# Kernel tuning notes

Hardware: AMD Instinct MI355X
Metric: run time of the kernel (lower is better)

The kernel has to match this reference:

```python
import jax, jax.numpy as jnp
import numpy as np

N_NODES = 50000
N_GRAPHS = 512


def gcn_conv(x, W, b, row, col, norm, n_nodes):
    # PyG GCNConv: h = x @ W; out_i = sum_{j->i} norm_ij * h_j + b
    h = x @ W  # [N, H]
    msgs = h[row] * norm[:, None]  # gather source features, scale
    out = jax.ops.segment_sum(msgs, col, num_segments=n_nodes)
    return out + b


def reference(x, edge_index, batch, W0, b0, W1, b1, W2, b2, Wf, bf):
    n = x.shape[0]
    src, dst = edge_index[0], edge_index[1]
    # add self loops
    loop = jnp.arange(n)
    row = jnp.concatenate([src, loop])
    col = jnp.concatenate([dst, loop])
    # symmetric degree normalization: 1/sqrt(deg_i * deg_j)
    deg = jax.ops.segment_sum(jnp.ones_like(col, dtype=x.dtype), col, num_segments=n)
    dis = jnp.where(deg > 0, 1.0 / jnp.sqrt(deg), 0.0)
    norm = dis[row] * dis[col]

    h = x
    for W, b in ((W0, b0), (W1, b1), (W2, b2)):
        h = jax.nn.relu(gcn_conv(h, W, b, row, col, norm, n))
        # dropout is identity in eval mode

    # global mean pool over graphs
    sums = jax.ops.segment_sum(h, batch, num_segments=N_GRAPHS)
    counts = jax.ops.segment_sum(jnp.ones((n,), dtype=h.dtype), batch, num_segments=N_GRAPHS)
    pooled = sums / jnp.maximum(counts, 1.0)[:, None]  # [B, H]

    logits = pooled @ Wf + bf
    return jax.nn.log_softmax(logits, axis=1)


def setup_inputs() -> dict:
    key = jax.random.key(0)
    ks = jax.random.split(key, 12)
    d_in, d_h, d_out = 128, 128, 10
    x = jax.random.normal(ks[0], (N_NODES, d_in), dtype=jnp.float32)
    edge_index = jax.random.randint(ks[1], (2, 600000), 0, N_NODES, dtype=jnp.int64)
    batch = jnp.sort(jax.random.randint(ks[2], (N_NODES,), 0, N_GRAPHS, dtype=jnp.int64))
    s = 1.0 / np.sqrt(d_h)
    return {
        "x": x,
        "edge_index": edge_index,
        "batch": batch,
        "W0": jax.random.normal(ks[3], (d_in, d_h), dtype=jnp.float32) * s,
        "b0": jnp.zeros((d_h,), dtype=jnp.float32),
        "W1": jax.random.normal(ks[4], (d_h, d_h), dtype=jnp.float32) * s,
        "b1": jnp.zeros((d_h,), dtype=jnp.float32),
        "W2": jax.random.normal(ks[5], (d_h, d_h), dtype=jnp.float32) * s,
        "b2": jnp.zeros((d_h,), dtype=jnp.float32),
        "Wf": jax.random.normal(ks[6], (d_h, d_out), dtype=jnp.float32) * s,
        "bf": jnp.zeros((d_out,), dtype=jnp.float32),
    }
```

## Files before the change

kernel.cpp:

```cpp
#include <hip/hip_runtime.h>
#include <hip/hip_bf16.h>

#define NN 50000
#define NE 600000
#define NG 512
#define DH 128

__global__ __launch_bounds__(256) void k_zero(float* p, int n) {
    int i = blockIdx.x * 256 + threadIdx.x;
    if (i < n) p[i] = 0.0f;
}

__global__ __launch_bounds__(256) void k_hist(const int* __restrict__ dst, int* __restrict__ deg) {
    int e = blockIdx.x * 256 + threadIdx.x;
    if (e < NE) atomicAdd(&deg[dst[e]], 1);
}

__global__ __launch_bounds__(256) void k_counts(const int* __restrict__ batch, float* __restrict__ counts) {
    int i = blockIdx.x * 256 + threadIdx.x;
    if (i < NN) atomicAdd(&counts[batch[i]], 1.0f);
}

__global__ __launch_bounds__(256) void k_alloc(const int* __restrict__ deg, int* __restrict__ gcur,
                                               int* __restrict__ rowstart, int* __restrict__ cursor,
                                               float* __restrict__ dis) {
    int i = blockIdx.x * 256 + threadIdx.x;
    if (i >= NN) return;
    int d = deg[i];
    int st = atomicAdd(gcur, d);
    rowstart[i] = st;
    cursor[i] = st;
    dis[i] = 1.0f / sqrtf((float)(d + 1));
}

__global__ __launch_bounds__(256) void k_fill(const int* __restrict__ src, const int* __restrict__ dst,
                                              const float* __restrict__ dis, int* __restrict__ cursor,
                                              int* __restrict__ csrc, float* __restrict__ cw) {
    int e = blockIdx.x * 256 + threadIdx.x;
    if (e >= NE) return;
    int s = src[e], d = dst[e];
    int slot = atomicAdd(&cursor[d], 1);
    csrc[slot] = s;
    cw[slot] = dis[s] * dis[d];
}

__global__ __launch_bounds__(256) void k_gemm128(const float* __restrict__ A,
                                                 const float* __restrict__ W,
                                                 float* __restrict__ C, int M) {
    __shared__ float As[64][20];
    __shared__ float Bs[16][132];
    int tid = threadIdx.x;
    int r0 = blockIdx.x * 64;
    int tr = tid >> 4, tc = tid & 15;

    float acc[4][8];
#pragma unroll
    for (int i = 0; i < 4; ++i)
#pragma unroll
        for (int j = 0; j < 8; ++j) acc[i][j] = 0.f;

    int arow = tid >> 2, ac4 = (tid & 3) * 4;

    for (int k0 = 0; k0 < 128; k0 += 16) {
        float4 av = make_float4(0.f, 0.f, 0.f, 0.f);
        int gr = r0 + arow;
        if (gr < M) av = *(const float4*)&A[gr * 128 + k0 + ac4];
        *(float4*)&As[arow][ac4] = av;
#pragma unroll
        for (int t = 0; t < 2; ++t) {
            int idx = tid + t * 256;
            int bk = idx >> 5, bc4 = (idx & 31) * 4;
            *(float4*)&Bs[bk][bc4] = *(const float4*)&W[(k0 + bk) * 128 + bc4];
        }
        __syncthreads();
#pragma unroll
        for (int kk = 0; kk < 16; ++kk) {
            float a[4];
#pragma unroll
            for (int i = 0; i < 4; ++i) a[i] = As[tr * 4 + i][kk];
            float4 bv0 = *(float4*)&Bs[kk][tc * 8];
            float4 bv1 = *(float4*)&Bs[kk][tc * 8 + 4];
            float b[8] = {bv0.x, bv0.y, bv0.z, bv0.w, bv1.x, bv1.y, bv1.z, bv1.w};
#pragma unroll
            for (int i = 0; i < 4; ++i)
#pragma unroll
                for (int j = 0; j < 8; ++j) acc[i][j] = fmaf(a[i], b[j], acc[i][j]);
        }
        __syncthreads();
    }

#pragma unroll
    for (int i = 0; i < 4; ++i) {
        int gr = r0 + tr * 4 + i;
        if (gr < M) {
            float4 o0 = make_float4(acc[i][0], acc[i][1], acc[i][2], acc[i][3]);
            float4 o1 = make_float4(acc[i][4], acc[i][5], acc[i][6], acc[i][7]);
            *(float4*)&C[gr * 128 + tc * 8] = o0;
            *(float4*)&C[gr * 128 + tc * 8 + 4] = o1;
        }
    }
}

template <int POOL>
__global__ __launch_bounds__(256) void k_gather(const float* __restrict__ h,
                                                const int* __restrict__ rowstart,
                                                const int* __restrict__ rowend,
                                                const int* __restrict__ csrc,
                                                const float* __restrict__ cw,
                                                const float* __restrict__ dis,
                                                const float* __restrict__ bias,
                                                float* __restrict__ outbuf,
                                                const int* __restrict__ batch,
                                                float* __restrict__ sums) {
    int t = blockIdx.x * 256 + threadIdx.x;
    int node = t >> 5;
    if (node >= NN) return;
    int f4 = t & 31;

    float d = dis[node];
    float w0 = d * d;
    float4 hv = ((const float4*)h)[node * 32 + f4];
    float4 acc = make_float4(hv.x * w0, hv.y * w0, hv.z * w0, hv.w * w0);

    int s = rowstart[node];
    int e = rowend[node];
    for (; s < e; ++s) {
        int sn = csrc[s];
        float w = cw[s];
        float4 v = ((const float4*)h)[sn * 32 + f4];
        acc.x = fmaf(v.x, w, acc.x);
        acc.y = fmaf(v.y, w, acc.y);
        acc.z = fmaf(v.z, w, acc.z);
        acc.w = fmaf(v.w, w, acc.w);
    }

    float4 b = ((const float4*)bias)[f4];
    acc.x = fmaxf(acc.x + b.x, 0.f);
    acc.y = fmaxf(acc.y + b.y, 0.f);
    acc.z = fmaxf(acc.z + b.z, 0.f);
    acc.w = fmaxf(acc.w + b.w, 0.f);

    if (POOL == 0) {
        ((float4*)outbuf)[node * 32 + f4] = acc;
    } else {
        int g = batch[node];
        float* o = sums + g * 128 + f4 * 4;
        atomicAdd(o + 0, acc.x);
        atomicAdd(o + 1, acc.y);
        atomicAdd(o + 2, acc.z);
        atomicAdd(o + 3, acc.w);
    }
}

__global__ __launch_bounds__(64) void k_head(const float* __restrict__ sums,
                                             const float* __restrict__ counts,
                                             const float* __restrict__ Wf,
                                             const float* __restrict__ bf,
                                             float* __restrict__ out) {
    int g = blockIdx.x;
    int l = threadIdx.x;
    float inv = 1.0f / fmaxf(counts[g], 1.0f);
    float p0 = sums[g * 128 + l] * inv;
    float p1 = sums[g * 128 + 64 + l] * inv;
    float logit[10];
#pragma unroll
    for (int o = 0; o < 10; ++o) {
        float part = p0 * Wf[l * 10 + o] + p1 * Wf[(l + 64) * 10 + o];
#pragma unroll
        for (int s = 32; s > 0; s >>= 1) part += __shfl_xor(part, s);
        logit[o] = part + bf[o];
    }
    if (l == 0) {
        float m = logit[0];
#pragma unroll
        for (int o = 1; o < 10; ++o) m = fmaxf(m, logit[o]);
        float sum = 0.f;
#pragma unroll
        for (int o = 0; o < 10; ++o) sum += expf(logit[o] - m);
        float lse = m + logf(sum);
#pragma unroll
        for (int o = 0; o < 10; ++o) out[g * 10 + o] = logit[o] - lse;
    }
}

extern "C" void kernel_launch(void* const* d_in, const int* in_sizes, int n_in,
                              void* d_out, int out_size, void* d_ws, size_t ws_size,
                              hipStream_t stream) {
    const float* x     = (const float*)d_in[0];
    const int*   ei    = (const int*)d_in[1];
    const int*   batch = (const int*)d_in[2];
    const float* W0 = (const float*)d_in[3];
    const float* b0 = (const float*)d_in[4];
    const float* W1 = (const float*)d_in[5];
    const float* b1 = (const float*)d_in[6];
    const float* W2 = (const float*)d_in[7];
    const float* b2 = (const float*)d_in[8];
    const float* Wf = (const float*)d_in[9];
    const float* bf = (const float*)d_in[10];
    float* out = (float*)d_out;

    float* ws = (float*)d_ws;
    float* sums    = ws;
    float* counts  = ws + 65536;
    int*   in_deg  = (int*)(ws + 66048);
    int*   gcur    = (int*)(ws + 116096);
    float* dis     = ws + 116160;
    int*   rowstart= (int*)(ws + 166208);
    int*   cursor  = (int*)(ws + 216256);
    int*   csr_src = (int*)(ws + 266304);
    float* csr_w   = ws + 866368;
    float* bufA    = ws + 1466432;
    float* bufB    = bufA + NN * DH;

    const int* src = ei;
    const int* dst = ei + NE;

    k_zero<<<(116160 + 255) / 256, 256, 0, stream>>>(ws, 116160);
    k_hist<<<2344, 256, 0, stream>>>(dst, in_deg);
    k_counts<<<196, 256, 0, stream>>>(batch, counts);
    k_alloc<<<196, 256, 0, stream>>>(in_deg, gcur, rowstart, cursor, dis);
    k_fill<<<2344, 256, 0, stream>>>(src, dst, dis, cursor, csr_src, csr_w);

    k_gemm128<<<(NN + 63) / 64, 256, 0, stream>>>(x, W0, bufB, NN);
    k_gather<0><<<6250, 256, 0, stream>>>(bufB, rowstart, cursor, csr_src, csr_w, dis, b0, bufA, batch, sums);

    k_gemm128<<<(NN + 63) / 64, 256, 0, stream>>>(bufA, W1, bufB, NN);
    k_gather<0><<<6250, 256, 0, stream>>>(bufB, rowstart, cursor, csr_src, csr_w, dis, b1, bufA, batch, sums);

    k_gemm128<<<(NN + 63) / 64, 256, 0, stream>>>(bufA, W2, bufB, NN);
    k_gather<1><<<6250, 256, 0, stream>>>(bufB, rowstart, cursor, csr_src, csr_w, dis, b2, nullptr, batch, sums);

    k_head<<<512, 64, 0, stream>>>(sums, counts, Wf, bf, out);
}
```

Before: 446.0 us.

## Store activations in bf16 and use MFMA bf16 GEMMs for GCN layers

Converts the input features and weights to bf16, replaces the fp32 SIMT GEMM with a bf16 MFMA 16x16x32 kernel that loads operands straight from global memory, and stores the intermediate hidden features in bf16. The gather kernels read bf16 rows, which halves the bytes moved in the edge-gather phase, and accumulate in fp32. The cost is an extra conversion pass over x and the weights, reduced precision in the intermediate activations, and scattered 2-byte stores from the GEMM epilogue.

```diff
diff --git a/kernel.cpp b/kernel.cpp
--- a/kernel.cpp
+++ b/kernel.cpp
@@ -4,7 +4,22 @@
 #define NN 50000
 #define NE 600000
 #define NG 512
-#define DH 128
+
+typedef __attribute__((ext_vector_type(8))) short bf16x8;
+typedef __attribute__((ext_vector_type(4))) float f32x4;
+
+__device__ __forceinline__ float bf_lo(unsigned u) {
+    unsigned v = u << 16;
+    return __builtin_bit_cast(float, v);
+}
+__device__ __forceinline__ float bf_hi(unsigned u) {
+    unsigned v = u & 0xFFFF0000u;
+    return __builtin_bit_cast(float, v);
+}
+__device__ __forceinline__ unsigned f2bf(float f) {
+    unsigned u = __builtin_bit_cast(unsigned, f);
+    return (u + 0x7FFFu + ((u >> 16) & 1u)) >> 16;
+}
 
 __global__ __launch_bounds__(256) void k_zero(float* p, int n) {
     int i = blockIdx.x * 256 + threadIdx.x;
@@ -44,111 +59,122 @@
     cw[slot] = dis[s] * dis[d];
 }
 
-__global__ __launch_bounds__(256) void k_gemm128(const float* __restrict__ A,
-                                                 const float* __restrict__ W,
-                                                 float* __restrict__ C, int M) {
-    __shared__ float As[64][20];
-    __shared__ float Bs[16][132];
-    int tid = threadIdx.x;
-    int r0 = blockIdx.x * 64;
-    int tr = tid >> 4, tc = tid & 15;
-
-    float acc[4][8];
-#pragma unroll
-    for (int i = 0; i < 4; ++i)
-#pragma unroll
-        for (int j = 0; j < 8; ++j) acc[i][j] = 0.f;
-
-    int arow = tid >> 2, ac4 = (tid & 3) * 4;
-
-    for (int k0 = 0; k0 < 128; k0 += 16) {
-        float4 av = make_float4(0.f, 0.f, 0.f, 0.f);
-        int gr = r0 + arow;
-        if (gr < M) av = *(const float4*)&A[gr * 128 + k0 + ac4];
-        *(float4*)&As[arow][ac4] = av;
-#pragma unroll
-        for (int t = 0; t < 2; ++t) {
-            int idx = tid + t * 256;
-            int bk = idx >> 5, bc4 = (idx & 31) * 4;
-            *(float4*)&Bs[bk][bc4] = *(const float4*)&W[(k0 + bk) * 128 + bc4];
+__global__ __launch_bounds__(256) void k_cvt_x(const float4* __restrict__ in, uint2* __restrict__ out, int n4) {
+    int i = blockIdx.x * 256 + threadIdx.x;
+    if (i >= n4) return;
+    float4 v = in[i];
+    uint2 o;
+    o.x = f2bf(v.x) | (f2bf(v.y) << 16);
+    o.y = f2bf(v.z) | (f2bf(v.w) << 16);
+    out[i] = o;
+}
+
+__global__ __launch_bounds__(256) void k_cvt_w(const float* __restrict__ W0, const float* __restrict__ W1,
+                                               const float* __restrict__ W2, unsigned short* __restrict__ Wt) {
+    int idx = blockIdx.x * 256 + threadIdx.x;
+    if (idx >= 3 * 16384) return;
+    int m = idx >> 14;
+    int r = idx & 16383;
+    int k = r >> 7, c = r & 127;
+    const float* W = (m == 0) ? W0 : (m == 1) ? W1 : W2;
+    Wt[m * 16384 + c * 128 + k] = (unsigned short)f2bf(W[k * 128 + c]);
+}
+
+__global__ __launch_bounds__(256) void k_gemm_mfma(const unsigned short* __restrict__ A,
+                                                   const unsigned short* __restrict__ Wt,
+                                                   unsigned short* __restrict__ C, int M) {
+    int wave = threadIdx.x >> 6;
+    int lane = threadIdx.x & 63;
+    int rowbase = blockIdx.x * 64 + wave * 16;
+    int lr = lane & 15;
+    int kg = lane >> 4;
+
+    int arow = rowbase + lr;
+    if (arow >= M) arow = M - 1;
+    bf16x8 a[4];
+#pragma unroll
+    for (int kt = 0; kt < 4; ++kt)
+        a[kt] = *(const bf16x8*)&A[arow * 128 + kt * 32 + kg * 8];
+
+    f32x4 acc[8];
+#pragma unroll
+    for (int nt = 0; nt < 8; ++nt) acc[nt] = (f32x4){0.f, 0.f, 0.f, 0.f};
+
+#pragma unroll
+    for (int nt = 0; nt < 8; ++nt) {
+        const unsigned short* wp = &Wt[(nt * 16 + lr) * 128 + kg * 8];
+#pragma unroll
+        for (int kt = 0; kt < 4; ++kt) {
+            bf16x8 b = *(const bf16x8*)&wp[kt * 32];
+            acc[nt] = __builtin_amdgcn_mfma_f32_16x16x32_bf16(a[kt], b, acc[nt], 0, 0, 0);
         }
-        __syncthreads();
-#pragma unroll
-        for (int kk = 0; kk < 16; ++kk) {
-            float a[4];
-#pragma unroll
-            for (int i = 0; i < 4; ++i) a[i] = As[tr * 4 + i][kk];
-            float4 bv0 = *(float4*)&Bs[kk][tc * 8];
-            float4 bv1 = *(float4*)&Bs[kk][tc * 8 + 4];
-            float b[8] = {bv0.x, bv0.y, bv0.z, bv0.w, bv1.x, bv1.y, bv1.z, bv1.w};
-#pragma unroll
-            for (int i = 0; i < 4; ++i)
-#pragma unroll
-                for (int j = 0; j < 8; ++j) acc[i][j] = fmaf(a[i], b[j], acc[i][j]);
+    }
+
+    int crow0 = rowbase + (lane >> 4) * 4;
+#pragma unroll
+    for (int nt = 0; nt < 8; ++nt) {
+#pragma unroll
+        for (int r = 0; r < 4; ++r) {
+            int gr = crow0 + r;
+            if (gr < M) C[gr * 128 + nt * 16 + lr] = (unsigned short)f2bf(acc[nt][r]);
         }
-        __syncthreads();
-    }
-
-#pragma unroll
-    for (int i = 0; i < 4; ++i) {
-        int gr = r0 + tr * 4 + i;
-        if (gr < M) {
-            float4 o0 = make_float4(acc[i][0], acc[i][1], acc[i][2], acc[i][3]);
-            float4 o1 = make_float4(acc[i][4], acc[i][5], acc[i][6], acc[i][7]);
-            *(float4*)&C[gr * 128 + tc * 8] = o0;
-            *(float4*)&C[gr * 128 + tc * 8 + 4] = o1;
-        }
     }
 }
 
 template <int POOL>
-__global__ __launch_bounds__(256) void k_gather(const float* __restrict__ h,
+__global__ __launch_bounds__(256) void k_gather(const uint2* __restrict__ h,
                                                 const int* __restrict__ rowstart,
                                                 const int* __restrict__ rowend,
                                                 const int* __restrict__ csrc,
                                                 const float* __restrict__ cw,
                                                 const float* __restrict__ dis,
                                                 const float* __restrict__ bias,
-                                                float* __restrict__ outbuf,
+                                                uint2* __restrict__ outbuf,
                                                 const int* __restrict__ batch,
                                                 float* __restrict__ sums) {
     int t = blockIdx.x * 256 + threadIdx.x;
     int node = t >> 5;
     if (node >= NN) return;
-    int f4 = t & 31;
+    int f = t & 31;
 
     float d = dis[node];
     float w0 = d * d;
-    float4 hv = ((const float4*)h)[node * 32 + f4];
-    float4 acc = make_float4(hv.x * w0, hv.y * w0, hv.z * w0, hv.w * w0);
+    uint2 hv = h[node * 32 + f];
+    float a0 = bf_lo(hv.x) * w0;
+    float a1 = bf_hi(hv.x) * w0;
+    float a2 = bf_lo(hv.y) * w0;
+    float a3 = bf_hi(hv.y) * w0;
 
     int s = rowstart[node];
     int e = rowend[node];
     for (; s < e; ++s) {
         int sn = csrc[s];
         float w = cw[s];
-        float4 v = ((const float4*)h)[sn * 32 + f4];
-        acc.x = fmaf(v.x, w, acc.x);
-        acc.y = fmaf(v.y, w, acc.y);
-        acc.z = fmaf(v.z, w, acc.z);
-        acc.w = fmaf(v.w, w, acc.w);
-    }
-
-    float4 b = ((const float4*)bias)[f4];
-    acc.x = fmaxf(acc.x + b.x, 0.f);
-    acc.y = fmaxf(acc.y + b.y, 0.f);
-    acc.z = fmaxf(acc.z + b.z, 0.f);
-    acc.w = fmaxf(acc.w + b.w, 0.f);
+        uint2 v = h[sn * 32 + f];
+        a0 = fmaf(bf_lo(v.x), w, a0);
+        a1 = fmaf(bf_hi(v.x), w, a1);
+        a2 = fmaf(bf_lo(v.y), w, a2);
+        a3 = fmaf(bf_hi(v.y), w, a3);
+    }
+
+    float4 b = ((const float4*)bias)[f];
+    a0 = fmaxf(a0 + b.x, 0.f);
+    a1 = fmaxf(a1 + b.y, 0.f);
+    a2 = fmaxf(a2 + b.z, 0.f);
+    a3 = fmaxf(a3 + b.w, 0.f);
 
     if (POOL == 0) {
-        ((float4*)outbuf)[node * 32 + f4] = acc;
+        uint2 o;
+        o.x = f2bf(a0) | (f2bf(a1) << 16);
+        o.y = f2bf(a2) | (f2bf(a3) << 16);
+        outbuf[node * 32 + f] = o;
     } else {
         int g = batch[node];
-        float* o = sums + g * 128 + f4 * 4;
-        atomicAdd(o + 0, acc.x);
-        atomicAdd(o + 1, acc.y);
-        atomicAdd(o + 2, acc.z);
-        atomicAdd(o + 3, acc.w);
+        float* o = sums + g * 128 + f * 4;
+        atomicAdd(o + 0, a0);
+        atomicAdd(o + 1, a1);
+        atomicAdd(o + 2, a2);
+        atomicAdd(o + 3, a3);
     }
 }
 
@@ -209,8 +235,10 @@
     int*   cursor  = (int*)(ws + 216256);
     int*   csr_src = (int*)(ws + 266304);
     float* csr_w   = ws + 866368;
-    float* bufA    = ws + 1466432;
-    float* bufB    = bufA + NN * DH;
+    unsigned short* Wt = (unsigned short*)(ws + 1466432);
+    unsigned short* bx = (unsigned short*)(ws + 1491008);
+    unsigned short* hA = (unsigned short*)(ws + 4691008);
+    unsigned short* hB = (unsigned short*)(ws + 7891008);
 
     const int* src = ei;
     const int* dst = ei + NE;
@@ -220,15 +248,20 @@
     k_counts<<<196, 256, 0, stream>>>(batch, counts);
     k_alloc<<<196, 256, 0, stream>>>(in_deg, gcur, rowstart, cursor, dis);
     k_fill<<<2344, 256, 0, stream>>>(src, dst, dis, cursor, csr_src, csr_w);
-
-    k_gemm128<<<(NN + 63) / 64, 256, 0, stream>>>(x, W0, bufB, NN);
-    k_gather<0><<<6250, 256, 0, stream>>>(bufB, rowstart, cursor, csr_src, csr_w, dis, b0, bufA, batch, sums);
-
-    k_gemm128<<<(NN + 63) / 64, 256, 0, stream>>>(bufA, W1, bufB, NN);
-    k_gather<0><<<6250, 256, 0, stream>>>(bufB, rowstart, cursor, csr_src, csr_w, dis, b1, bufA, batch, sums);
-
-    k_gemm128<<<(NN + 63) / 64, 256, 0, stream>>>(bufA, W2, bufB, NN);
-    k_gather<1><<<6250, 256, 0, stream>>>(bufB, rowstart, cursor, csr_src, csr_w, dis, b2, nullptr, batch, sums);
+    k_cvt_x<<<6250, 256, 0, stream>>>((const float4*)x, (uint2*)bx, NN * 32);
+    k_cvt_w<<<192, 256, 0, stream>>>(W0, W1, W2, Wt);
+
+    const int GEMM_GRID = (NN + 63) / 64;
+
+    k_gemm_mfma<<<GEMM_GRID, 256, 0, stream>>>(bx, Wt, hB, NN);
+    k_gather<0><<<6250, 256, 0, stream>>>((const uint2*)hB, rowstart, cursor, csr_src, csr_w,
+                                          dis, b0, (uint2*)hA, batch, sums);
+    k_gemm_mfma<<<GEMM_GRID, 256, 0, stream>>>(hA, Wt + 16384, hB, NN);
+    k_gather<0><<<6250, 256, 0, stream>>>((const uint2*)hB, rowstart, cursor, csr_src, csr_w,
+                                          dis, b1, (uint2*)hA, batch, sums);
+    k_gemm_mfma<<<GEMM_GRID, 256, 0, stream>>>(hA, Wt + 32768, hB, NN);
+    k_gather<1><<<6250, 256, 0, stream>>>((const uint2*)hB, rowstart, cursor, csr_src, csr_w,
+                                          dis, b2, nullptr, batch, sums);
 
     k_head<<<512, 64, 0, stream>>>(sums, counts, Wf, bf, out);
 }
```

After: 408.2 us. 8.5% less time.
